# Performance work log

Hardware: AMD Instinct MI355X
Metric: run time of the kernel (lower is better)

## Reference

```python
import jax, jax.numpy as jnp
import numpy as np

B, T, C = 8, 2048, 1024      # batch, timesteps, input_dim
G, E = 2, 320                # groups_dim, entries_dim
EMB = 512                    # emb_dim
D = EMB // G                 # true_emb_dim per group


def setup_inputs() -> dict:
    key = jax.random.key(0)
    k1, k2, k3 = jax.random.split(key, 3)
    X = jax.random.normal(k1, (B, T, C), dtype=jnp.float32)
    # nn.Linear(input_dim, G*E): weight (out,in) ~ N(0,1), bias zeros
    W = jax.random.normal(k2, (G * E, C), dtype=jnp.float32)
    b = jnp.zeros((G * E,), dtype=jnp.float32)
    # codebook Parameter(1, G*E, D) ~ U[0,1); stored squeezed as (G*E, D)
    codebook = jax.random.uniform(k3, (G * E, D), dtype=jnp.float32)
    return {"X": X, "W": W, "b": b, "codebook": codebook}


def reference(X, W, b, codebook):
    # Eval-mode forward of VectorQuantization (time_first=True).
    nB, nT, _ = X.shape
    logits = jnp.einsum("btc,kc->btk", X, W) + b           # (B, T, G*E)
    # Faithful to source: view (B,T,G*E) as (B*G, T*E) and argmax over last dim
    flat = logits.reshape(nB * G, nT * E)                   # (B*G, T*E)
    k = jnp.argmax(flat, axis=-1)                           # (B*G,)
    hard = jax.nn.one_hot(k, nT * E, dtype=logits.dtype)    # (B*G, T*E)
    q = hard.reshape(nB * nT, G, E)                         # (B*T, G, E)
    # (one-hot * codebook).sum over entries == per-group gather
    cb = codebook.reshape(G, E, D)                          # (G, E, D)
    out = jnp.einsum("nge,ged->ngd", q, cb)                 # (B*T, G, D)
    return out.reshape(nB, nT, G * D)                       # (B, T, emb_dim)
```

## Files before the change

kernel.cpp:

```cpp
#include <hip/hip_runtime.h>
#include <stdint.h>

#define CC    1024
#define EE    320
#define KN    640
#define DD    256
#define MTOT  16384
#define NBLK  640
#define OUT4  2097152
#define ZPB   3277
#define MARGIN 2.0f

typedef __attribute__((ext_vector_type(8))) short short8;
typedef __attribute__((ext_vector_type(4))) float f32x4;

__device__ __forceinline__ unsigned int f32_orderable(float x) {
    unsigned int b = __float_as_uint(x);
    return (b & 0x80000000u) ? ~b : (b | 0x80000000u);
}

__device__ __forceinline__ unsigned short bf16_rne(float x) {
    unsigned int u = __float_as_uint(x);
    return (unsigned short)((u + 0x7FFFu + ((u >> 16) & 1u)) >> 16);
}

__global__ void init_slots_kernel(unsigned long long* __restrict__ slots) {
    if (threadIdx.x < 17) slots[threadIdx.x] = 0ull;
}

__global__ __launch_bounds__(256)
void prep_kernel(const float* __restrict__ W, unsigned short* __restrict__ B2F,
                 unsigned long long* __restrict__ slots) {
    if (blockIdx.x == 0 && threadIdx.x < 17) slots[threadIdx.x] = 0ull;
    const int lane = threadIdx.x & 63;
    int unit = blockIdx.x * 4 + (threadIdx.x >> 6);
    int rt = unit >> 5, kc = unit & 31;
    int row = rt * 16 + (lane & 15);
    int col = kc * 32 + ((lane >> 4) << 3);
    const float* p = W + (size_t)row * CC + col;
    float4 v0 = *(const float4*)p;
    float4 v1 = *(const float4*)(p + 4);
    short8 hi;
    hi[0] = (short)bf16_rne(v0.x); hi[1] = (short)bf16_rne(v0.y);
    hi[2] = (short)bf16_rne(v0.z); hi[3] = (short)bf16_rne(v0.w);
    hi[4] = (short)bf16_rne(v1.x); hi[5] = (short)bf16_rne(v1.y);
    hi[6] = (short)bf16_rne(v1.z); hi[7] = (short)bf16_rne(v1.w);
    *(short8*)(B2F + (size_t)unit * 512 + lane * 8) = hi;
}

__global__ __launch_bounds__(256, 3)
void vq_fused(const float* __restrict__ X,
              const unsigned short* __restrict__ B2F,
              const float* __restrict__ W,
              const float* __restrict__ bias,
              const float* __restrict__ codebook,
              float* __restrict__ out,
              unsigned long long* __restrict__ slots,
              unsigned int* __restrict__ counter) {
    __shared__ __align__(16) unsigned short lds_s[16384];
    __shared__ float redf[4];
    __shared__ int cnt_s;
    __shared__ int cand_s[128];
    __shared__ unsigned int done_s;
    __shared__ unsigned long long s16[16];

    const int tid  = threadIdx.x;
    const int lane = tid & 63;
    const int wave = tid >> 6;

    const int l   = blockIdx.x;
    const int xcd = l & 7;
    const int w   = l >> 3;
    const int mt  = xcd * 16 + w / 5;
    const int nt  = w % 5;
    const int m0  = mt * 128;
    const int n0  = nt * 128;
    const int wm  = (wave >> 1) * 64;
    const int wn  = (wave & 1) * 64;

    char* ldsb = (char*)lds_s;

    const int r  = tid >> 1;
    const int hh = tid & 1;
    const float* gA = X + (size_t)(m0 + r) * CC + hh * 16;
    const int wAoff = (r >> 4) * 1024 + (r & 15) * 16 + hh * 512;
    const unsigned short* gB0 = B2F + (size_t)((nt * 8 + 2 * wave) * 32) * 512 + lane * 8;
    const unsigned short* gB1 = B2F + (size_t)((nt * 8 + 2 * wave + 1) * 32) * 512 + lane * 8;
    const int u0off = 8192 + (2 * wave) * 1024;
    const int u1off = u0off + 1024;
    const int aoff = (wm >> 4) * 1024 + lane * 16;
    const int boff = 8192 + (wn >> 4) * 1024 + lane * 16;

    f32x4 acc[4][4] = {};
    float4 fa0, fa1, fa2, fa3;

#define CVTPK(d, lo, hi) asm("v_cvt_pk_bf16_f32 %0, %1, %2" : "=v"(d) : "v"(lo), "v"(hi))

#define STAGE_ISSUE(T, BB)                                                               \
    {                                                                                    \
        const float* ga_ = gA + (size_t)(T) * 32;                                        \
        fa0 = *(const float4*)(ga_);                                                     \
        fa1 = *(const float4*)(ga_ + 4);                                                 \
        fa2 = *(const float4*)(ga_ + 8);                                                 \
        fa3 = *(const float4*)(ga_ + 12);                                                \
        __builtin_amdgcn_global_load_lds(                                                \
            (const __attribute__((address_space(1))) void*)(gB0 + (size_t)(T) * 512),    \
            (__attribute__((address_space(3))) void*)(ldsb + (BB) + u0off), 16, 0, 0);   \
        __builtin_amdgcn_global_load_lds(                                                \
            (const __attribute__((address_space(1))) void*)(gB1 + (size_t)(T) * 512),    \
            (__attribute__((address_space(3))) void*)(ldsb + (BB) + u1off), 16, 0, 0);   \
    }

#define STAGE_WRITE(BB)                                                                  \
    {                                                                                    \
        unsigned int c0, c1, c2, c3, c4, c5, c6, c7;                                     \
        CVTPK(c0, fa0.x, fa0.y); CVTPK(c1, fa0.z, fa0.w);                                \
        CVTPK(c2, fa1.x, fa1.y); CVTPK(c3, fa1.z, fa1.w);                                \
        CVTPK(c4, fa2.x, fa2.y); CVTPK(c5, fa2.z, fa2.w);                                \
        CVTPK(c6, fa3.x, fa3.y); CVTPK(c7, fa3.z, fa3.w);                                \
        *(int4*)(ldsb + (BB) + wAoff)       = make_int4((int)c0, (int)c1, (int)c2, (int)c3); \
        *(int4*)(ldsb + (BB) + wAoff + 256) = make_int4((int)c4, (int)c5, (int)c6, (int)c7); \
    }

#define COMPUTE(BB)                                                                      \
    {                                                                                    \
        short8 af[4], bfr[4];                                                            \
        _Pragma("unroll")                                                                \
        for (int t = 0; t < 4; t++) {                                                    \
            af[t]  = *(const short8*)(ldsb + (BB) + aoff + t * 1024);                    \
            bfr[t] = *(const short8*)(ldsb + (BB) + boff + t * 1024);                    \
        }                                                                                \
        _Pragma("unroll")                                                                \
        for (int ti = 0; ti < 4; ti++)                                                   \
            _Pragma("unroll")                                                            \
            for (int tj = 0; tj < 4; tj++)                                               \
                acc[ti][tj] = __builtin_amdgcn_mfma_f32_16x16x32_bf16(                   \
                    af[ti], bfr[tj], acc[ti][tj], 0, 0, 0);                              \
    }

    STAGE_ISSUE(0, 0)
    {
        int base = l * ZPB;
        f32x4 z = {0.f, 0.f, 0.f, 0.f};
        for (int j = 0; j < 13; j++) {
            int o = j * 256 + tid;
            int idx = base + o;
            if (o < ZPB && idx < OUT4)
                __builtin_nontemporal_store(z, (f32x4*)out + idx);
        }
    }
    STAGE_WRITE(0)
    asm volatile("s_waitcnt vmcnt(0)" ::: "memory");
    __syncthreads();

    for (int it = 0; it < 16; it++) {
        STAGE_ISSUE(2 * it + 1, 16384)
        COMPUTE(0)
        STAGE_WRITE(16384)
        asm volatile("s_waitcnt vmcnt(0)" ::: "memory");
        __syncthreads();
        if (it < 15) {
            STAGE_ISSUE(2 * it + 2, 0)
            COMPUTE(16384)
            STAGE_WRITE(0)
            asm volatile("s_waitcnt vmcnt(0)" ::: "memory");
        } else {
            COMPUTE(16384)
        }
        __syncthreads();
    }

#undef COMPUTE
#undef STAGE_WRITE
#undef STAGE_ISSUE
#undef CVTPK

    float bias4[4];
#pragma unroll
    for (int tj = 0; tj < 4; tj++) bias4[tj] = bias[n0 + wn + tj * 16 + (lane & 15)];

    float vmax = -3.0e38f;
#pragma unroll
    for (int ti = 0; ti < 4; ti++)
#pragma unroll
        for (int tj = 0; tj < 4; tj++)
#pragma unroll
            for (int rr = 0; rr < 4; rr++)
                vmax = fmaxf(vmax, acc[ti][tj][rr] + bias4[tj]);
#pragma unroll
    for (int off = 32; off > 0; off >>= 1)
        vmax = fmaxf(vmax, __shfl_down(vmax, off, 64));
    if (lane == 0) redf[wave] = vmax;
    if (tid == 0) cnt_s = 0;
    __syncthreads();
    float bm = fmaxf(fmaxf(redf[0], redf[1]), fmaxf(redf[2], redf[3]));
    float thresh = bm - MARGIN;

#pragma unroll
    for (int ti = 0; ti < 4; ti++) {
#pragma unroll
        for (int rr = 0; rr < 4; rr++) {
            int m = m0 + wm + ti * 16 + (lane >> 4) * 4 + rr;
#pragma unroll
            for (int tj = 0; tj < 4; tj++) {
                float v = acc[ti][tj][rr] + bias4[tj];
                if (v >= thresh) {
                    int n = n0 + wn + tj * 16 + (lane & 15);
                    int idx = atomicAdd(&cnt_s, 1);
                    if (idx < 128) cand_s[idx] = (m << 10) | n;
                }
            }
        }
    }
    __syncthreads();
    int cnt = cnt_s < 128 ? cnt_s : 128;

    for (int i = 0; i < cnt; i++) {
        int mc = cand_s[i] >> 10;
        int nc = cand_s[i] & 1023;
        float4 xv = *(const float4*)(X + (size_t)mc * CC + tid * 4);
        float4 wv = *(const float4*)(W + (size_t)nc * CC + tid * 4);
        float p = xv.x * wv.x + xv.y * wv.y + xv.z * wv.z + xv.w * wv.w;
#pragma unroll
        for (int off = 32; off > 0; off >>= 1) p += __shfl_down(p, off, 64);
        if (lane == 0) redf[wave] = p;
        __syncthreads();
        if (tid == 0) {
            float tot = redf[0] + redf[1] + redf[2] + redf[3] + bias[nc];
            unsigned int c = (unsigned int)((mc & 1023) * KN + nc);
            unsigned long long pk =
                ((unsigned long long)f32_orderable(tot) << 32) |
                (unsigned long long)(~c);
            atomicMax(slots + (mc >> 10), pk);
        }
        __syncthreads();
    }

    if (tid == 0) {
        __threadfence();
        done_s = atomicAdd(counter, 1u);
    }
    __syncthreads();

    if (done_s == NBLK - 1) {
        if (tid < 16) s16[tid] = atomicAdd(slots + tid, 0ull);
        __syncthreads();
        int rr  = tid >> 4;
        int seg = tid & 15;
        unsigned long long p = s16[rr];
        unsigned int c = ~(unsigned int)(p & 0xFFFFFFFFull);
        int tl = (int)(c / KN);
        int kg = (int)(c % KN);
        int b  = rr >> 1, h = rr & 1;
        int nstar = b * 2048 + h * 1024 + tl;
        int g = kg / EE;
        const float4* src = (const float4*)(codebook + (size_t)kg * DD) + seg * 4;
        float4* dst = (float4*)(out + (size_t)nstar * 512 + (size_t)g * DD) + seg * 4;
#pragma unroll
        for (int j = 0; j < 4; j++) dst[j] = src[j];
    }
}

__global__ __launch_bounds__(256)
void zs_kernel(const unsigned long long* __restrict__ slots,
               const float* __restrict__ codebook,
               float4* __restrict__ out4) {
    int i4 = blockIdx.x * 256 + threadIdx.x;
    int n  = i4 >> 7;
    int c4 = i4 & 127;
    int b  = n >> 11;
    int h  = (n >> 10) & 1;
    unsigned long long p = slots[b * 2 + h];
    unsigned int c = ~(unsigned int)(p & 0xFFFFFFFFull);
    int tl = (int)(c / KN);
    int kg = (int)(c % KN);
    int nstar = b * 2048 + h * 1024 + tl;
    int g = kg / EE;
    float4 v = make_float4(0.f, 0.f, 0.f, 0.f);
    if (n == nstar && (c4 >> 6) == g)
        v = ((const float4*)codebook)[kg * 64 + (c4 & 63)];
    out4[i4] = v;
}

#define BM 128
#define BN 64
#define BK 32
#define LDA (BM + 4)
#define LDB (BN + 4)

__global__ __launch_bounds__(128)
void gemm_argmax_f32(const float* __restrict__ X, const float* __restrict__ W,
                     const float* __restrict__ bias,
                     unsigned long long* __restrict__ slots) {
    __shared__ float Asf[BK][LDA];
    __shared__ float Bsf[BK][LDB];
    const int tid = threadIdx.x;
    const int m0 = blockIdx.y * BM;
    const int n0 = blockIdx.x * BN;
    const int tx = tid & 7, ty = tid >> 3;
    float acc[8][8];
#pragma unroll
    for (int i = 0; i < 8; i++)
#pragma unroll
        for (int j = 0; j < 8; j++) acc[i][j] = 0.0f;
    const int lm = tid >> 3, lk = (tid & 7) * 4;
    const float* Xb = X + (size_t)m0 * CC;
    const float* Wb = W + (size_t)n0 * CC;
    for (int k0 = 0; k0 < CC; k0 += BK) {
#pragma unroll
        for (int rr = 0; rr < 8; rr++) {
            int m = rr * 16 + lm;
            float4 v = *(const float4*)(Xb + (size_t)m * CC + k0 + lk);
            Asf[lk + 0][m] = v.x; Asf[lk + 1][m] = v.y; Asf[lk + 2][m] = v.z; Asf[lk + 3][m] = v.w;
        }
#pragma unroll
        for (int rr = 0; rr < 4; rr++) {
            int m = rr * 16 + lm;
            float4 v = *(const float4*)(Wb + (size_t)m * CC + k0 + lk);
            Bsf[lk + 0][m] = v.x; Bsf[lk + 1][m] = v.y; Bsf[lk + 2][m] = v.z; Bsf[lk + 3][m] = v.w;
        }
        __syncthreads();
#pragma unroll
        for (int kk = 0; kk < BK; kk++) {
            float4 A0 = *(const float4*)&Asf[kk][ty * 8];
            float4 A1 = *(const float4*)&Asf[kk][ty * 8 + 4];
            float4 B0 = *(const float4*)&Bsf[kk][tx * 8];
            float4 B1 = *(const float4*)&Bsf[kk][tx * 8 + 4];
            float a[8] = {A0.x, A0.y, A0.z, A0.w, A1.x, A1.y, A1.z, A1.w};
            float b[8] = {B0.x, B0.y, B0.z, B0.w, B1.x, B1.y, B1.z, B1.w};
#pragma unroll
            for (int i = 0; i < 8; i++)
#pragma unroll
                for (int j = 0; j < 8; j++) acc[i][j] = fmaf(a[i], b[j], acc[i][j]);
        }
        __syncthreads();
    }
    unsigned long long best = 0ull;
#pragma unroll
    for (int i = 0; i < 8; i++) {
        int mg = m0 + ty * 8 + i;
        int tl = mg & 1023;
#pragma unroll
        for (int j = 0; j < 8; j++) {
            int kg = n0 + tx * 8 + j;
            float v = acc[i][j] + bias[kg];
            unsigned int c = (unsigned int)(tl * KN + kg);
            unsigned long long p = ((unsigned long long)f32_orderable(v) << 32) |
                                   (unsigned long long)(~c);
            if (p > best) best = p;
        }
    }
#pragma unroll
    for (int off = 32; off > 0; off >>= 1) {
        unsigned long long o = __shfl_down(best, off, 64);
        if (o > best) best = o;
    }
    __shared__ unsigned long long red2[2];
    if ((tid & 63) == 0) red2[tid >> 6] = best;
    __syncthreads();
    if (tid == 0) {
        unsigned long long b0 = red2[0], b1 = red2[1];
        atomicMax(slots + (m0 >> 10), b0 > b1 ? b0 : b1);
    }
}

extern "C" void kernel_launch(void* const* d_in, const int* in_sizes, int n_in,
                              void* d_out, int out_size, void* d_ws, size_t ws_size,
                              hipStream_t stream) {
    const float* X        = (const float*)d_in[0];
    const float* W        = (const float*)d_in[1];
    const float* bias     = (const float*)d_in[2];
    const float* codebook = (const float*)d_in[3];
    float* out = (float*)d_out;

    unsigned long long* slots = (unsigned long long*)d_ws;
    unsigned int* counter = (unsigned int*)(slots + 16);
    const size_t B_off   = 256;
    const size_t B_bytes = (size_t)KN * CC * 2;
    const size_t need = B_off + B_bytes;

    if (ws_size >= need) {
        unsigned short* B2F = (unsigned short*)((char*)d_ws + B_off);
        hipLaunchKernelGGL(prep_kernel, dim3(320), dim3(256), 0, stream, W, B2F, slots);
        hipLaunchKernelGGL(vq_fused, dim3(NBLK), dim3(256), 0, stream,
                           X, B2F, W, bias, codebook, out, slots, counter);
    } else {
        hipLaunchKernelGGL(init_slots_kernel, dim3(1), dim3(64), 0, stream, slots);
        hipLaunchKernelGGL(gemm_argmax_f32, dim3(KN / BN, MTOT / BM), dim3(128), 0, stream,
                           X, W, bias, slots);
        hipLaunchKernelGGL(zs_kernel, dim3(OUT4 / 256), dim3(256), 0, stream,
                           slots, codebook, (float4*)out);
    }
}
```

Before: 173.2 us.

## Replace LDS-staged GEMM with direct-to-register multi-stage global loads

Removes the shared-memory staging of X and packed W tiles. Each wave now loads its own A and B MFMA fragments straight from global memory into registers, using a 3-deep A and 2-deep B register prefetch ring in a fully unrolled K loop. This drops the LDS writes, LDS reads and block barriers from the main loop. In exchange, data that was shared across waves through LDS is now loaded redundantly from global or L2 memory. Register pressure rises, so the occupancy hint is lowered from 3 to 2 blocks per CU.

```diff
diff --git a/kernel.cpp b/kernel.cpp
--- a/kernel.cpp
+++ b/kernel.cpp
@@ -13,6 +13,7 @@
 
 typedef __attribute__((ext_vector_type(8))) short short8;
 typedef __attribute__((ext_vector_type(4))) float f32x4;
+typedef __attribute__((ext_vector_type(4))) int   i32x4;
 
 __device__ __forceinline__ unsigned int f32_orderable(float x) {
     unsigned int b = __float_as_uint(x);
@@ -48,7 +49,7 @@
     *(short8*)(B2F + (size_t)unit * 512 + lane * 8) = hi;
 }
 
-__global__ __launch_bounds__(256, 3)
+__global__ __launch_bounds__(256, 2)
 void vq_fused(const float* __restrict__ X,
               const unsigned short* __restrict__ B2F,
               const float* __restrict__ W,
@@ -57,7 +58,6 @@
               float* __restrict__ out,
               unsigned long long* __restrict__ slots,
               unsigned int* __restrict__ counter) {
-    __shared__ __align__(16) unsigned short lds_s[16384];
     __shared__ float redf[4];
     __shared__ int cnt_s;
     __shared__ int cand_s[128];
@@ -78,67 +78,39 @@
     const int wm  = (wave >> 1) * 64;
     const int wn  = (wave & 1) * 64;
 
-    char* ldsb = (char*)lds_s;
-
-    const int r  = tid >> 1;
-    const int hh = tid & 1;
-    const float* gA = X + (size_t)(m0 + r) * CC + hh * 16;
-    const int wAoff = (r >> 4) * 1024 + (r & 15) * 16 + hh * 512;
-    const unsigned short* gB0 = B2F + (size_t)((nt * 8 + 2 * wave) * 32) * 512 + lane * 8;
-    const unsigned short* gB1 = B2F + (size_t)((nt * 8 + 2 * wave + 1) * 32) * 512 + lane * 8;
-    const int u0off = 8192 + (2 * wave) * 1024;
-    const int u1off = u0off + 1024;
-    const int aoff = (wm >> 4) * 1024 + lane * 16;
-    const int boff = 8192 + (wn >> 4) * 1024 + lane * 16;
+    const float* Ap[4];
+#pragma unroll
+    for (int f = 0; f < 4; f++)
+        Ap[f] = X + (size_t)(m0 + wm + f * 16 + (lane & 15)) * CC + ((lane >> 4) << 3);
+    const unsigned short* Bq[4];
+#pragma unroll
+    for (int f = 0; f < 4; f++)
+        Bq[f] = B2F + ((size_t)(((n0 + wn) >> 4) + f) * 32) * 512 + lane * 8;
 
     f32x4 acc[4][4] = {};
-    float4 fa0, fa1, fa2, fa3;
-
-#define CVTPK(d, lo, hi) asm("v_cvt_pk_bf16_f32 %0, %1, %2" : "=v"(d) : "v"(lo), "v"(hi))
-
-#define STAGE_ISSUE(T, BB)                                                               \
-    {                                                                                    \
-        const float* ga_ = gA + (size_t)(T) * 32;                                        \
-        fa0 = *(const float4*)(ga_);                                                     \
-        fa1 = *(const float4*)(ga_ + 4);                                                 \
-        fa2 = *(const float4*)(ga_ + 8);                                                 \
-        fa3 = *(const float4*)(ga_ + 12);                                                \
-        __builtin_amdgcn_global_load_lds(                                                \
-            (const __attribute__((address_space(1))) void*)(gB0 + (size_t)(T) * 512),    \
-            (__attribute__((address_space(3))) void*)(ldsb + (BB) + u0off), 16, 0, 0);   \
-        __builtin_amdgcn_global_load_lds(                                                \
-            (const __attribute__((address_space(1))) void*)(gB1 + (size_t)(T) * 512),    \
-            (__attribute__((address_space(3))) void*)(ldsb + (BB) + u1off), 16, 0, 0);   \
-    }
-
-#define STAGE_WRITE(BB)                                                                  \
-    {                                                                                    \
-        unsigned int c0, c1, c2, c3, c4, c5, c6, c7;                                     \
-        CVTPK(c0, fa0.x, fa0.y); CVTPK(c1, fa0.z, fa0.w);                                \
-        CVTPK(c2, fa1.x, fa1.y); CVTPK(c3, fa1.z, fa1.w);                                \
-        CVTPK(c4, fa2.x, fa2.y); CVTPK(c5, fa2.z, fa2.w);                                \
-        CVTPK(c6, fa3.x, fa3.y); CVTPK(c7, fa3.z, fa3.w);                                \
-        *(int4*)(ldsb + (BB) + wAoff)       = make_int4((int)c0, (int)c1, (int)c2, (int)c3); \
-        *(int4*)(ldsb + (BB) + wAoff + 256) = make_int4((int)c4, (int)c5, (int)c6, (int)c7); \
-    }
-
-#define COMPUTE(BB)                                                                      \
-    {                                                                                    \
-        short8 af[4], bfr[4];                                                            \
-        _Pragma("unroll")                                                                \
-        for (int t = 0; t < 4; t++) {                                                    \
-            af[t]  = *(const short8*)(ldsb + (BB) + aoff + t * 1024);                    \
-            bfr[t] = *(const short8*)(ldsb + (BB) + boff + t * 1024);                    \
-        }                                                                                \
-        _Pragma("unroll")                                                                \
-        for (int ti = 0; ti < 4; ti++)                                                   \
-            _Pragma("unroll")                                                            \
-            for (int tj = 0; tj < 4; tj++)                                               \
-                acc[ti][tj] = __builtin_amdgcn_mfma_f32_16x16x32_bf16(                   \
-                    af[ti], bfr[tj], acc[ti][tj], 0, 0, 0);                              \
-    }
-
-    STAGE_ISSUE(0, 0)
+    float4 As[3][4][2];
+    short8 Bs[2][4];
+
+#define LOADA(S, T)                                                          \
+    {                                                                        \
+        _Pragma("unroll")                                                    \
+        for (int f = 0; f < 4; f++) {                                        \
+            As[S][f][0] = *(const float4*)(Ap[f] + (T) * 32);                \
+            As[S][f][1] = *(const float4*)(Ap[f] + (T) * 32 + 4);            \
+        }                                                                    \
+    }
+#define LOADB(S, T)                                                          \
+    {                                                                        \
+        _Pragma("unroll")                                                    \
+        for (int f = 0; f < 4; f++)                                          \
+            Bs[S][f] = *(const short8*)(Bq[f] + (size_t)(T) * 512);          \
+    }
+
+    LOADA(0, 0)
+    LOADB(0, 0)
+    LOADA(1, 1)
+    LOADB(1, 1)
+    LOADA(2, 2)
     {
         int base = l * ZPB;
         f32x4 z = {0.f, 0.f, 0.f, 0.f};
@@ -149,31 +121,36 @@
                 __builtin_nontemporal_store(z, (f32x4*)out + idx);
         }
     }
-    STAGE_WRITE(0)
-    asm volatile("s_waitcnt vmcnt(0)" ::: "memory");
-    __syncthreads();
-
-    for (int it = 0; it < 16; it++) {
-        STAGE_ISSUE(2 * it + 1, 16384)
-        COMPUTE(0)
-        STAGE_WRITE(16384)
-        asm volatile("s_waitcnt vmcnt(0)" ::: "memory");
-        __syncthreads();
-        if (it < 15) {
-            STAGE_ISSUE(2 * it + 2, 0)
-            COMPUTE(16384)
-            STAGE_WRITE(0)
-            asm volatile("s_waitcnt vmcnt(0)" ::: "memory");
-        } else {
-            COMPUTE(16384)
-        }
-        __syncthreads();
-    }
-
-#undef COMPUTE
-#undef STAGE_WRITE
-#undef STAGE_ISSUE
+
+#define CVTPK(d, lo, hi) asm("v_cvt_pk_bf16_f32 %0, %1, %2" : "=v"(d) : "v"(lo), "v"(hi))
+
+#pragma unroll
+    for (int t = 0; t < 32; t++) {
+        const int ia = t % 3;
+        const int ib = t % 2;
+        short8 af[4];
+#pragma unroll
+        for (int f = 0; f < 4; f++) {
+            unsigned c0, c1, c2, c3;
+            CVTPK(c0, As[ia][f][0].x, As[ia][f][0].y);
+            CVTPK(c1, As[ia][f][0].z, As[ia][f][0].w);
+            CVTPK(c2, As[ia][f][1].x, As[ia][f][1].y);
+            CVTPK(c3, As[ia][f][1].z, As[ia][f][1].w);
+            i32x4 pk = {(int)c0, (int)c1, (int)c2, (int)c3};
+            af[f] = *(short8*)&pk;
+        }
+        if (t + 3 < 32) LOADA(ia, t + 3)
+#pragma unroll
+        for (int ti = 0; ti < 4; ti++)
+#pragma unroll
+            for (int tj = 0; tj < 4; tj++)
+                acc[ti][tj] = __builtin_amdgcn_mfma_f32_16x16x32_bf16(
+                    af[ti], Bs[ib][tj], acc[ti][tj], 0, 0, 0);
+        if (t + 2 < 32) LOADB(ib, t + 2)
+    }
 #undef CVTPK
+#undef LOADA
+#undef LOADB
 
     float bias4[4];
 #pragma unroll
```

Result: slower. 259.9 us (+50.1%).
